# Performance work log

Measured on AMD Instinct MI355X. Metric: run time of the kernel, lower is better.

Reference implementation:

```python
import jax, jax.numpy as jnp
import numpy as np

HEADS = 8
DIM_HEAD = 64
NB_FEATURES = 256
DIM = 512

def setup_inputs() -> dict:
    key = jax.random.key(0)
    ks = jax.random.split(key, 4)
    b, n = 2, 8192
    x = jax.random.normal(ks[0], (b, n, DIM), jnp.float32)
    # fan-in scaling so exp(feature projections) stays numerically sane
    Wqkv = jax.random.normal(ks[1], (3 * HEADS * DIM_HEAD, DIM), jnp.float32) / np.sqrt(DIM).astype(np.float32)
    Wout = jax.random.normal(ks[2], (DIM, HEADS * DIM_HEAD), jnp.float32) / np.sqrt(HEADS * DIM_HEAD).astype(np.float32)
    bout = jnp.zeros((DIM,), jnp.float32)
    proj = jax.random.normal(ks[3], (NB_FEATURES, DIM_HEAD), jnp.float32) / np.sqrt(DIM_HEAD).astype(np.float32)
    return {"x": x, "Wqkv": Wqkv, "Wout": Wout, "bout": bout, "proj": proj}

def reference(x, Wqkv, Wout, bout, proj):
    b, n, _ = x.shape
    scale = DIM_HEAD ** -0.5
    qkv = jnp.einsum('bnd,ed->bne', x, Wqkv)            # [b,n,3*h*dh]
    q, k, v = jnp.split(qkv, 3, axis=-1)
    to_heads = lambda t: t.reshape(b, n, HEADS, DIM_HEAD).transpose(0, 2, 1, 3)  # [b,h,n,dh]
    q = to_heads(q) * scale
    k = to_heads(k)
    v = to_heads(v)
    # FAVOR+ exp feature maps
    q_prime = jnp.exp(jnp.einsum('bhnd,fd->bhnf', q, proj))  # [b,h,n,f]
    k_prime = jnp.exp(jnp.einsum('bhnd,fd->bhnf', k, proj))  # [b,h,n,f]
    k_sum = k_prime.sum(axis=2)                              # [b,h,f]
    D = jnp.einsum('bhnf,bhf->bhn', q_prime, k_sum)          # normalizer
    D_inv = 1.0 / (D + 1e-6)
    context = jnp.einsum('bhmf,bhmd->bhfd', k_prime, v)      # [b,h,f,dh]
    out = jnp.einsum('bhnf,bhfd->bhnd', q_prime, context) * D_inv[..., None]
    out = out.transpose(0, 2, 1, 3).reshape(b, n, HEADS * DIM_HEAD)
    return jnp.einsum('bne,de->bnd', out, Wout) + bout
```

## Files before the change

### kernel.cpp

```cpp
#include <hip/hip_runtime.h>
#include <math.h>

#define B_    2
#define NSEQ  8192
#define DIM_  512
#define H_    8
#define DH_   64
#define F_    256
#define M_    (B_*NSEQ)
#define QKV_  1536

typedef __attribute__((ext_vector_type(8))) short     short8;
typedef __attribute__((ext_vector_type(4))) float     float4v;
typedef __attribute__((ext_vector_type(8))) unsigned short ushort8v;

__device__ __forceinline__ unsigned short f2bf(float f) {
    unsigned u = __float_as_uint(f);
    u += 0x7FFFu + ((u >> 16) & 1u);
    return (unsigned short)(u >> 16);
}
__device__ __forceinline__ float bf2f(unsigned short h) {
    unsigned u = ((unsigned)h) << 16;
    return __uint_as_float(u);
}
__device__ __forceinline__ unsigned pack2bf(float lo, float hi) {
    return __builtin_amdgcn_perm(__float_as_uint(hi), __float_as_uint(lo), 0x07060302);
}
__device__ __forceinline__ void glds16(const void* g, void* s) {
    __builtin_amdgcn_global_load_lds(
        (const __attribute__((address_space(1))) unsigned int*)g,
        (__attribute__((address_space(3))) unsigned int*)s, 16, 0, 0);
}

__global__ __launch_bounds__(256) void cvt_all(const float* __restrict__ x,
                                               const float* __restrict__ wqkv,
                                               const float* __restrict__ wout,
                                               const float* __restrict__ proj,
                                               unsigned short* __restrict__ xb,
                                               unsigned short* __restrict__ wqkvb,
                                               unsigned short* __restrict__ woutb,
                                               unsigned short* __restrict__ projb) {
    int bid = blockIdx.x;
    const float* in; unsigned short* out; int i;
    if (bid < 4096)      { in = x;    out = xb;    i = bid * 256 + threadIdx.x; }
    else if (bid < 4480) { in = wqkv; out = wqkvb; i = (bid - 4096) * 256 + threadIdx.x; }
    else if (bid < 4608) { in = wout; out = woutb; i = (bid - 4480) * 256 + threadIdx.x; }
    else                 { in = proj; out = projb; i = (bid - 4608) * 256 + threadIdx.x; }
    float4 a = ((const float4*)in)[2 * i];
    float4 b = ((const float4*)in)[2 * i + 1];
    ushort8v o;
    o[0] = f2bf(a.x); o[1] = f2bf(a.y); o[2] = f2bf(a.z); o[3] = f2bf(a.w);
    o[4] = f2bf(b.x); o[5] = f2bf(b.y); o[6] = f2bf(b.z); o[7] = f2bf(b.w);
    ((ushort8v*)out)[i] = o;
}

template<bool BF16OUT>
__global__ __launch_bounds__(256) void gemm_nt_pp(const unsigned short* __restrict__ A,
                                                  const unsigned short* __restrict__ Bm,
                                                  const float* __restrict__ bias,
                                                  void* __restrict__ Cout,
                                                  unsigned short* __restrict__ vTout,
                                                  int M, int N, int K) {
    __shared__ __align__(16) unsigned short As[3][128 * 32];
    __shared__ __align__(16) unsigned short Bs[3][128 * 32];
    const int t  = threadIdx.x;
    const int w  = t >> 6, l = t & 63;
    const int wm = w >> 1, wn = w & 1;
    const int lr = l & 15, lq = l >> 4;

    const int gx = gridDim.x;
    int flat = blockIdx.y * gx + blockIdx.x;
    int per  = (gx * gridDim.y) >> 3;
    int flat2 = (flat & 7) * per + (flat >> 3);
    const int m0 = (flat2 / gx) * 128, n0 = (flat2 % gx) * 128;

    float4v acc[4][4];
#pragma unroll
    for (int mi = 0; mi < 4; mi++)
#pragma unroll
        for (int ni = 0; ni < 4; ni++) acc[mi][ni] = (float4v){0.f, 0.f, 0.f, 0.f};

    auto stage = [&](int buf, int k0) {
#pragma unroll
        for (int i = 0; i < 2; i++) {
            int rb8 = w * 2 + i;
            int row = rb8 * 16 + lr;
            glds16(A + (size_t)(m0 + row) * K + k0 + lq * 8, &As[buf][rb8 * 512]);
            glds16(Bm + (size_t)(n0 + row) * K + k0 + lq * 8, &Bs[buf][rb8 * 512]);
        }
    };

    const int nk = K >> 5;
    stage(0, 0);
    stage(1, 32);

    for (int k = 0; k < nk; k++) {
        if (k + 1 < nk) { asm volatile("s_waitcnt vmcnt(4)" ::: "memory"); }
        else            { asm volatile("s_waitcnt vmcnt(0)" ::: "memory"); }
        __builtin_amdgcn_s_barrier();

        const int cur = k % 3;
        if (k + 2 < nk) stage((k + 2) % 3, (k + 2) << 5);

        short8 af[4], bfr[4];
#pragma unroll
        for (int mi = 0; mi < 4; mi++)
            af[mi] = *(const short8*)&As[cur][((wm * 4 + mi) * 64 + l) * 8];
#pragma unroll
        for (int ni = 0; ni < 4; ni++)
            bfr[ni] = *(const short8*)&Bs[cur][((wn * 4 + ni) * 64 + l) * 8];

        __builtin_amdgcn_s_setprio(1);
#pragma unroll
        for (int mi = 0; mi < 4; mi++)
#pragma unroll
            for (int ni = 0; ni < 4; ni++)
                acc[mi][ni] = __builtin_amdgcn_mfma_f32_16x16x32_bf16(
                    af[mi], bfr[ni], acc[mi][ni], 0, 0, 0);
        __builtin_amdgcn_s_setprio(0);
    }

    const int q = l >> 4, c = l & 15;
#pragma unroll
    for (int mi = 0; mi < 4; mi++) {
        int row0 = m0 + wm * 64 + mi * 16 + q * 4;
#pragma unroll
        for (int ni = 0; ni < 4; ni++) {
            int col = n0 + wn * 64 + ni * 16 + c;
            if (BF16OUT && vTout != nullptr && col >= 1024) {
                int cm = col - 1024;
                int h2 = cm >> 6, dh = cm & 63;
                int bq = row0 >> 13;
                size_t nn = (size_t)(row0 & 8191);
                unsigned short* dst = vTout + (((size_t)bq * 8 + h2) * 64 + dh) * NSEQ + nn;
                uint2 pv;
                pv.x = ((unsigned)f2bf(acc[mi][ni][1]) << 16) | f2bf(acc[mi][ni][0]);
                pv.y = ((unsigned)f2bf(acc[mi][ni][3]) << 16) | f2bf(acc[mi][ni][2]);
                *(uint2*)dst = pv;
            } else {
                float bv = bias ? bias[col] : 0.f;
#pragma unroll
                for (int r = 0; r < 4; r++) {
                    float v = acc[mi][ni][r] + bv;
                    if (BF16OUT) ((unsigned short*)Cout)[(size_t)(row0 + r) * N + col] = f2bf(v);
                    else         ((float*)Cout)[(size_t)(row0 + r) * N + col] = v;
                }
            }
        }
    }
}

__global__ __launch_bounds__(512) void gemm_out_256(const unsigned short* __restrict__ A,
                                                    const unsigned short* __restrict__ Bm,
                                                    const float* __restrict__ bias,
                                                    float* __restrict__ Cout,
                                                    int M, int N, int K) {
    __shared__ __align__(16) unsigned short As[3][32 * 512];
    __shared__ __align__(16) unsigned short Bs[3][16 * 512];
    const int t  = threadIdx.x;
    const int w  = t >> 6, l = t & 63;
    const int wm = w >> 1, wn = w & 1;
    const int lr = l & 15, lq = l >> 4;

    const int gx = gridDim.x;
    int flat = blockIdx.y * gx + blockIdx.x;
    int per  = (gx * gridDim.y) >> 3;
    int flat2 = (flat & 7) * per + (flat >> 3);
    const int m0 = (flat2 / gx) * 256, n0 = (flat2 % gx) * 128;

    float4v acc[4][4];
#pragma unroll
    for (int mi = 0; mi < 4; mi++)
#pragma unroll
        for (int ni = 0; ni < 4; ni++) acc[mi][ni] = (float4v){0.f, 0.f, 0.f, 0.f};

    auto stage = [&](int buf, int k0) {
#pragma unroll
        for (int i = 0; i < 4; i++) {
            int c = w * 4 + i, rb = c >> 1, ks = c & 1;
            glds16(A + (size_t)(m0 + rb * 16 + lr) * K + k0 + ks * 32 + lq * 8,
                   &As[buf][c * 512]);
        }
#pragma unroll
        for (int i = 0; i < 2; i++) {
            int c = w * 2 + i, rb = c >> 1, ks = c & 1;
            glds16(Bm + (size_t)(n0 + rb * 16 + lr) * K + k0 + ks * 32 + lq * 8,
                   &Bs[buf][c * 512]);
        }
    };

    stage(0, 0);
    stage(1, 64);

#pragma unroll
    for (int k = 0; k < 8; k++) {
        if (k < 7) { asm volatile("s_waitcnt vmcnt(6)" ::: "memory"); }
        else       { asm volatile("s_waitcnt vmcnt(0)" ::: "memory"); }
        __builtin_amdgcn_s_barrier();
        const int cur = k % 3;

        if (k + 2 < 8) stage((k + 2) % 3, (k + 2) << 6);

        short8 af[2][4], bfr[2][4];
#pragma unroll
        for (int ks = 0; ks < 2; ks++) {
#pragma unroll
            for (int mi = 0; mi < 4; mi++)
                af[ks][mi] = *(const short8*)&As[cur][(((wm * 4 + mi) * 2 + ks) * 64 + l) * 8];
#pragma unroll
            for (int ni = 0; ni < 4; ni++)
                bfr[ks][ni] = *(const short8*)&Bs[cur][(((wn * 4 + ni) * 2 + ks) * 64 + l) * 8];
        }

        __builtin_amdgcn_s_setprio(1);
#pragma unroll
        for (int ks = 0; ks < 2; ks++)
#pragma unroll
            for (int mi = 0; mi < 4; mi++)
#pragma unroll
                for (int ni = 0; ni < 4; ni++)
                    acc[mi][ni] = __builtin_amdgcn_mfma_f32_16x16x32_bf16(
                        af[ks][mi], bfr[ks][ni], acc[mi][ni], 0, 0, 0);
        __builtin_amdgcn_s_setprio(0);
    }

    const int q = l >> 4, c = l & 15;
#pragma unroll
    for (int mi = 0; mi < 4; mi++) {
        int row0 = m0 + wm * 64 + mi * 16 + q * 4;
#pragma unroll
        for (int ni = 0; ni < 4; ni++) {
            int col = n0 + wn * 64 + ni * 16 + c;
            float bv = bias ? bias[col] : 0.f;
#pragma unroll
            for (int r = 0; r < 4; r++)
                Cout[(size_t)(row0 + r) * N + col] = acc[mi][ni][r] + bv;
        }
    }
}

__global__ __launch_bounds__(256) void ctx_fused_mfma(
    const unsigned short* __restrict__ qkvb,
    const unsigned short* __restrict__ projb,
    const unsigned short* __restrict__ vT,
    unsigned short* __restrict__ partial)
{
    __shared__ __align__(16) unsigned short PB[16 * 512];
    __shared__ __align__(16) unsigned short KB[8 * 512];
    __shared__ __align__(16) unsigned short VB[8 * 512];
    __shared__ __align__(16) unsigned short KPA[16 * 512];
    const int t = threadIdx.x, w = t >> 6, l = t & 63;
    const int lr = l & 15, lq = l >> 4;
    const int s = blockIdx.x, fh = blockIdx.y, z = blockIdx.z;
    const int b = z >> 3, h = z & 7;
    const int nchunk = s * 512;

    for (int idx = w; idx < 16; idx += 4) {
        int fblk = idx >> 1, kt = idx & 1;
        glds16(projb + (size_t)(fh * 128 + fblk * 16 + lr) * 64 + kt * 32 + lq * 8, &PB[idx * 512]);
    }

    float4v acc[2][5];
#pragma unroll
    for (int mi = 0; mi < 2; mi++)
#pragma unroll
        for (int ni = 0; ni < 5; ni++) acc[mi][ni] = (float4v){0.f, 0.f, 0.f, 0.f};
    short ov = (lr == 0) ? (short)0x3F80 : (short)0;
    short8 ones = {ov, ov, ov, ov, ov, ov, ov, ov};

    for (int st = 0; st < 8; st++) {
        int nbase = nchunk + st * 64;
        __syncthreads();
        for (int idx = w; idx < 8; idx += 4) {
            int nblk = idx >> 1, kt = idx & 1;
            glds16(qkvb + ((size_t)b * NSEQ + nbase + nblk * 16 + lr) * QKV_ + 512 + h * 64 + kt * 32 + lq * 8,
                   &KB[idx * 512]);
        }
        for (int idx = w; idx < 8; idx += 4) {
            int dhb = idx >> 1, nt2 = idx & 1;
            glds16(vT + ((size_t)z * 64 + dhb * 16 + lr) * NSEQ + nbase + nt2 * 32 + lq * 8,
                   &VB[idx * 512]);
        }
        __syncthreads();

        float4v a2[4][2];
#pragma unroll
        for (int mi = 0; mi < 4; mi++)
#pragma unroll
            for (int ni = 0; ni < 2; ni++) a2[mi][ni] = (float4v){0.f, 0.f, 0.f, 0.f};
#pragma unroll
        for (int ks = 0; ks < 2; ks++) {
            short8 ka[4], pb[2];
#pragma unroll
            for (int mi = 0; mi < 4; mi++)
                ka[mi] = *(const short8*)&KB[((mi * 2 + ks) * 64 + l) * 8];
#pragma unroll
            for (int ni = 0; ni < 2; ni++)
                pb[ni] = *(const short8*)&PB[(((w * 2 + ni) * 2 + ks) * 64 + l) * 8];
#pragma unroll
            for (int mi = 0; mi < 4; mi++)
#pragma unroll
                for (int ni = 0; ni < 2; ni++)
                    a2[mi][ni] = __builtin_amdgcn_mfma_f32_16x16x32_bf16(ka[mi], pb[ni], a2[mi][ni], 0, 0, 0);
        }
#pragma unroll
        for (int mi = 0; mi < 4; mi++) {
            int nb = mi * 16 + lq * 4;
            int qoff = ((nb >> 3) & 3) * 256 + (nb & 7) * 2;
            int setn = nb >> 5;
#pragma unroll
            for (int ni = 0; ni < 2; ni++) {
                int fp = w * 32 + ni * 16 + lr;
                float e0 = __expf(a2[mi][ni][0]);
                float e1 = __expf(a2[mi][ni][1]);
                float e2 = __expf(a2[mi][ni][2]);
                float e3 = __expf(a2[mi][ni][3]);
                uint2 p; p.x = pack2bf(e0, e1); p.y = pack2bf(e2, e3);
                *(uint2*)((char*)KPA + (size_t)(((fp >> 4) * 2 + setn) * 1024 + qoff + (fp & 15) * 16)) = p;
            }
        }
#pragma unroll
        for (int ks = 0; ks < 2; ks++) {
            short8 af[2], bf[4];
#pragma unroll
            for (int mi = 0; mi < 2; mi++)
                af[mi] = *(const short8*)&KPA[(((w * 2 + mi) * 2 + ks) * 64 + l) * 8];
#pragma unroll
            for (int ni = 0; ni < 4; ni++)
                bf[ni] = *(const short8*)&VB[((ni * 2 + ks) * 64 + l) * 8];
#pragma unroll
            for (int mi = 0; mi < 2; mi++) {
#pragma unroll
                for (int ni = 0; ni < 4; ni++)
                    acc[mi][ni] = __builtin_amdgcn_mfma_f32_16x16x32_bf16(af[mi], bf[ni], acc[mi][ni], 0, 0, 0);
                acc[mi][4] = __builtin_amdgcn_mfma_f32_16x16x32_bf16(af[mi], ones, acc[mi][4], 0, 0, 0);
            }
        }
    }
    unsigned short* base = partial + (size_t)(s * 16 + z) * 80 * 256 + fh * 128;
#pragma unroll
    for (int mi = 0; mi < 2; mi++) {
        int f0r = w * 32 + mi * 16 + lq * 4;
#pragma unroll
        for (int ni = 0; ni < 5; ni++) {
            int col = ni * 16 + lr;
#pragma unroll
            for (int r = 0; r < 4; r++)
                base[(size_t)col * 256 + f0r + r] = f2bf(acc[mi][ni][r]);
        }
    }
}

__global__ __launch_bounds__(256) void ctx_reduce(const unsigned short* __restrict__ partial,
                                                  unsigned short* __restrict__ ctxT) {
    int idx2 = blockIdx.x * 256 + threadIdx.x;
    const int INNER = 16 * 80 * 256;
    size_t off = (size_t)idx2 * 2;
    float s0 = 0.f, s1 = 0.f;
#pragma unroll
    for (int k = 0; k < 16; k++) {
        unsigned v = *(const unsigned*)(partial + (size_t)k * INNER + off);
        s0 += bf2f((unsigned short)(v & 0xffffu));
        s1 += bf2f((unsigned short)(v >> 16));
    }
    *(unsigned*)(ctxT + off) = ((unsigned)f2bf(s1) << 16) | f2bf(s0);
}

__global__ __launch_bounds__(256) void attn_fused_mfma(
    const unsigned short* __restrict__ qkvb,
    const unsigned short* __restrict__ projb,
    const unsigned short* __restrict__ ctxT,
    unsigned short* __restrict__ attnb)
{
    __shared__ __align__(16) unsigned short QB[16 * 512];
    __shared__ __align__(16) unsigned short PA[8 * 512];
    __shared__ __align__(16) unsigned short QPA[16 * 512];
    __shared__ __align__(16) unsigned short CB[10 * 512];
    const int t = threadIdx.x, w = t >> 6, l = t & 63;
    const int lr = l & 15, lq = l >> 4;
    const int m0 = blockIdx.x * 128, z = blockIdx.y;
    const int b = z >> 3, h = z & 7;

    for (int idx = w; idx < 16; idx += 4) {
        int mblk = idx >> 1, kt = idx & 1;
        glds16(qkvb + ((size_t)b * NSEQ + m0 + mblk * 16 + lr) * QKV_ + h * 64 + kt * 32 + lq * 8,
               &QB[idx * 512]);
    }
    float4v acc[2][5];
#pragma unroll
    for (int mi = 0; mi < 2; mi++)
#pragma unroll
        for (int ni = 0; ni < 5; ni++) acc[mi][ni] = (float4v){0.f, 0.f, 0.f, 0.f};

    for (int fs = 0; fs < 4; fs++) {
        int f0 = fs * 64;
        __syncthreads();
        for (int idx = w; idx < 8; idx += 4) {
            int fb = idx >> 1, kt = idx & 1;
            glds16(projb + (size_t)(f0 + fb * 16 + lr) * 64 + kt * 32 + lq * 8, &PA[idx * 512]);
        }
        for (int idx = w; idx < 10; idx += 4) {
            int dhb = idx >> 1, ft = idx & 1;
            glds16(ctxT + ((size_t)z * 80 + dhb * 16 + lr) * 256 + f0 + ft * 32 + lq * 8,
                   &CB[idx * 512]);
        }
        __syncthreads();

        float4v a2[4][2];
#pragma unroll
        for (int mi = 0; mi < 4; mi++)
#pragma unroll
            for (int ni = 0; ni < 2; ni++) a2[mi][ni] = (float4v){0.f, 0.f, 0.f, 0.f};
#pragma unroll
        for (int ks = 0; ks < 2; ks++) {
            short8 pa[4], qb[2];
#pragma unroll
            for (int mi = 0; mi < 4; mi++)
                pa[mi] = *(const short8*)&PA[((mi * 2 + ks) * 64 + l) * 8];
#pragma unroll
            for (int ni = 0; ni < 2; ni++)
                qb[ni] = *(const short8*)&QB[(((w * 2 + ni) * 2 + ks) * 64 + l) * 8];
#pragma unroll
            for (int mi = 0; mi < 4; mi++)
#pragma unroll
                for (int ni = 0; ni < 2; ni++)
                    a2[mi][ni] = __builtin_amdgcn_mfma_f32_16x16x32_bf16(pa[mi], qb[ni], a2[mi][ni], 0, 0, 0);
        }
#pragma unroll
        for (int mi = 0; mi < 4; mi++) {
            int fb2 = mi * 16 + lq * 4;
            int qoff = ((fb2 >> 3) & 3) * 256 + (fb2 & 7) * 2;
            int setf = fb2 >> 5;
#pragma unroll
            for (int ni = 0; ni < 2; ni++) {
                int m = w * 32 + ni * 16 + lr;
                float e0 = __expf(0.125f * a2[mi][ni][0]);
                float e1 = __expf(0.125f * a2[mi][ni][1]);
                float e2 = __expf(0.125f * a2[mi][ni][2]);
                float e3 = __expf(0.125f * a2[mi][ni][3]);
                uint2 p; p.x = pack2bf(e0, e1); p.y = pack2bf(e2, e3);
                *(uint2*)((char*)QPA + (size_t)(((m >> 4) * 2 + setf) * 1024 + qoff + (m & 15) * 16)) = p;
            }
        }
#pragma unroll
        for (int ks = 0; ks < 2; ks++) {
            short8 af[2], cb[5];
#pragma unroll
            for (int mi = 0; mi < 2; mi++)
                af[mi] = *(const short8*)&QPA[(((w * 2 + mi) * 2 + ks) * 64 + l) * 8];
#pragma unroll
            for (int ni = 0; ni < 5; ni++)
                cb[ni] = *(const short8*)&CB[((ni * 2 + ks) * 64 + l) * 8];
#pragma unroll
            for (int mi = 0; mi < 2; mi++)
#pragma unroll
                for (int ni = 0; ni < 5; ni++)
                    acc[mi][ni] = __builtin_amdgcn_mfma_f32_16x16x32_bf16(af[mi], cb[ni], acc[mi][ni], 0, 0, 0);
        }
    }
#pragma unroll
    for (int mi = 0; mi < 2; mi++) {
        int rowb = m0 + w * 32 + mi * 16 + lq * 4;
#pragma unroll
        for (int r = 0; r < 4; r++) {
            float dv = __shfl(acc[mi][4][r], (l & 48), 64);
            float rinv = 1.f / (dv + 1e-6f);
#pragma unroll
            for (int ni = 0; ni < 4; ni++)
                attnb[((size_t)b * NSEQ + rowb + r) * 512 + h * 64 + ni * 16 + lr] =
                    f2bf(acc[mi][ni][r] * rinv);
        }
    }
}

extern "C" void kernel_launch(void* const* d_in, const int* in_sizes, int n_in,
                              void* d_out, int out_size, void* d_ws, size_t ws_size,
                              hipStream_t stream) {
    const float* x    = (const float*)d_in[0];
    const float* Wqkv = (const float*)d_in[1];
    const float* Wout = (const float*)d_in[2];
    const float* bout = (const float*)d_in[3];
    const float* proj = (const float*)d_in[4];

    unsigned short* qkvb    = (unsigned short*)d_ws;
    unsigned short* vT      = qkvb + (size_t)M_ * QKV_;
    unsigned short* partial = vT + (size_t)16 * 64 * NSEQ;
    unsigned short* ctxT    = partial + (size_t)16 * 16 * 80 * 256;
    unsigned short* projb   = ctxT + (size_t)16 * 80 * 256;
    unsigned short* xb      = projb + 16384;
    unsigned short* attnb   = xb;
    unsigned short* wqkvb   = xb + (size_t)M_ * DIM_;
    unsigned short* woutb   = wqkvb + (size_t)QKV_ * DIM_;
    float* outp = (float*)d_out;

    cvt_all<<<dim3(4616), 256, 0, stream>>>(x, Wqkv, Wout, proj, xb, wqkvb, woutb, projb);
    gemm_nt_pp<true><<<dim3(QKV_ / 128, M_ / 128), 256, 0, stream>>>(xb, wqkvb, nullptr, qkvb, vT, M_, QKV_, DIM_);
    ctx_fused_mfma<<<dim3(16, 2, 16), 256, 0, stream>>>(qkvb, projb, vT, partial);
    ctx_reduce<<<dim3(640), 256, 0, stream>>>(partial, ctxT);
    attn_fused_mfma<<<dim3(64, 16), 256, 0, stream>>>(qkvb, projb, ctxT, attnb);
    gemm_out_256<<<dim3(DIM_ / 128, M_ / 256), 512, 0, stream>>>(attnb, woutb, bout, outp, M_, DIM_, DIM_);
}
```

Before: 211.4 us.

## Deepen GEMM pipeline to five stages and double-buffer attention kernel loads

The GEMM kernel moves from a 3-buffer to a 5-buffer LDS ring, prefetching four K-tiles ahead with adjusted vmcnt waits. The context and output attention kernels double-buffer their K/V and proj/ctx tiles, so the next chunk's global-to-LDS copy is issued while the current chunk is computed. This is meant to hide global memory latency, at the cost of more shared memory per block, which may lower occupancy. In the attention kernels the wait is still vmcnt(0) at the top of each iteration, so the overlap reaches only across one compute phase.

```diff
diff --git a/kernel.cpp b/kernel.cpp
--- a/kernel.cpp
+++ b/kernel.cpp
@@ -61,8 +61,8 @@
                                                   void* __restrict__ Cout,
                                                   unsigned short* __restrict__ vTout,
                                                   int M, int N, int K) {
-    __shared__ __align__(16) unsigned short As[3][128 * 32];
-    __shared__ __align__(16) unsigned short Bs[3][128 * 32];
+    __shared__ __align__(16) unsigned short As[5][128 * 32];
+    __shared__ __align__(16) unsigned short Bs[5][128 * 32];
     const int t  = threadIdx.x;
     const int w  = t >> 6, l = t & 63;
     const int wm = w >> 1, wn = w & 1;
@@ -93,14 +93,18 @@
     const int nk = K >> 5;
     stage(0, 0);
     stage(1, 32);
+    stage(2, 64);
+    stage(3, 96);
 
     for (int k = 0; k < nk; k++) {
-        if (k + 1 < nk) { asm volatile("s_waitcnt vmcnt(4)" ::: "memory"); }
-        else            { asm volatile("s_waitcnt vmcnt(0)" ::: "memory"); }
+        if (k + 3 < nk)      { asm volatile("s_waitcnt vmcnt(12)" ::: "memory"); }
+        else if (k + 2 < nk) { asm volatile("s_waitcnt vmcnt(8)"  ::: "memory"); }
+        else if (k + 1 < nk) { asm volatile("s_waitcnt vmcnt(4)"  ::: "memory"); }
+        else                 { asm volatile("s_waitcnt vmcnt(0)"  ::: "memory"); }
         __builtin_amdgcn_s_barrier();
 
-        const int cur = k % 3;
-        if (k + 2 < nk) stage((k + 2) % 3, (k + 2) << 5);
+        const int cur = k % 5;
+        if (k + 4 < nk) stage((k + 4) % 5, (k + 4) << 5);
 
         short8 af[4], bfr[4];
 #pragma unroll
@@ -246,8 +250,8 @@
     unsigned short* __restrict__ partial)
 {
     __shared__ __align__(16) unsigned short PB[16 * 512];
-    __shared__ __align__(16) unsigned short KB[8 * 512];
-    __shared__ __align__(16) unsigned short VB[8 * 512];
+    __shared__ __align__(16) unsigned short KB[2][8 * 512];
+    __shared__ __align__(16) unsigned short VB[2][8 * 512];
     __shared__ __align__(16) unsigned short KPA[16 * 512];
     const int t = threadIdx.x, w = t >> 6, l = t & 63;
     const int lr = l & 15, lq = l >> 4;
@@ -255,10 +259,24 @@
     const int b = z >> 3, h = z & 7;
     const int nchunk = s * 512;
 
+    auto stageKV = [&](int bi, int nbase) {
+        for (int idx = w; idx < 8; idx += 4) {
+            int nblk = idx >> 1, kt = idx & 1;
+            glds16(qkvb + ((size_t)b * NSEQ + nbase + nblk * 16 + lr) * QKV_ + 512 + h * 64 + kt * 32 + lq * 8,
+                   &KB[bi][idx * 512]);
+        }
+        for (int idx = w; idx < 8; idx += 4) {
+            int dhb = idx >> 1, nt2 = idx & 1;
+            glds16(vT + ((size_t)z * 64 + dhb * 16 + lr) * NSEQ + nbase + nt2 * 32 + lq * 8,
+                   &VB[bi][idx * 512]);
+        }
+    };
+
     for (int idx = w; idx < 16; idx += 4) {
         int fblk = idx >> 1, kt = idx & 1;
         glds16(projb + (size_t)(fh * 128 + fblk * 16 + lr) * 64 + kt * 32 + lq * 8, &PB[idx * 512]);
     }
+    stageKV(0, nchunk);
 
     float4v acc[2][5];
 #pragma unroll
@@ -269,19 +287,11 @@
     short8 ones = {ov, ov, ov, ov, ov, ov, ov, ov};
 
     for (int st = 0; st < 8; st++) {
-        int nbase = nchunk + st * 64;
-        __syncthreads();
-        for (int idx = w; idx < 8; idx += 4) {
-            int nblk = idx >> 1, kt = idx & 1;
-            glds16(qkvb + ((size_t)b * NSEQ + nbase + nblk * 16 + lr) * QKV_ + 512 + h * 64 + kt * 32 + lq * 8,
-                   &KB[idx * 512]);
-        }
-        for (int idx = w; idx < 8; idx += 4) {
-            int dhb = idx >> 1, nt2 = idx & 1;
-            glds16(vT + ((size_t)z * 64 + dhb * 16 + lr) * NSEQ + nbase + nt2 * 32 + lq * 8,
-                   &VB[idx * 512]);
-        }
-        __syncthreads();
+        asm volatile("s_waitcnt vmcnt(0)" ::: "memory");
+        __builtin_amdgcn_s_barrier();
+        asm volatile("" ::: "memory");
+        const int cur = st & 1;
+        if (st < 7) stageKV(cur ^ 1, nchunk + (st + 1) * 64);
 
         float4v a2[4][2];
 #pragma unroll
@@ -293,7 +303,7 @@
             short8 ka[4], pb[2];
 #pragma unroll
             for (int mi = 0; mi < 4; mi++)
-                ka[mi] = *(const short8*)&KB[((mi * 2 + ks) * 64 + l) * 8];
+                ka[mi] = *(const short8*)&KB[cur][((mi * 2 + ks) * 64 + l) * 8];
 #pragma unroll
             for (int ni = 0; ni < 2; ni++)
                 pb[ni] = *(const short8*)&PB[(((w * 2 + ni) * 2 + ks) * 64 + l) * 8];
@@ -327,7 +337,7 @@
                 af[mi] = *(const short8*)&KPA[(((w * 2 + mi) * 2 + ks) * 64 + l) * 8];
 #pragma unroll
             for (int ni = 0; ni < 4; ni++)
-                bf[ni] = *(const short8*)&VB[((ni * 2 + ks) * 64 + l) * 8];
+                bf[ni] = *(const short8*)&VB[cur][((ni * 2 + ks) * 64 + l) * 8];
 #pragma unroll
             for (int mi = 0; mi < 2; mi++) {
 #pragma unroll
@@ -373,19 +383,33 @@
     unsigned short* __restrict__ attnb)
 {
     __shared__ __align__(16) unsigned short QB[16 * 512];
-    __shared__ __align__(16) unsigned short PA[8 * 512];
+    __shared__ __align__(16) unsigned short PA[2][8 * 512];
     __shared__ __align__(16) unsigned short QPA[16 * 512];
-    __shared__ __align__(16) unsigned short CB[10 * 512];
+    __shared__ __align__(16) unsigned short CB[2][10 * 512];
     const int t = threadIdx.x, w = t >> 6, l = t & 63;
     const int lr = l & 15, lq = l >> 4;
     const int m0 = blockIdx.x * 128, z = blockIdx.y;
     const int b = z >> 3, h = z & 7;
 
+    auto stagePC = [&](int bi, int f0n) {
+        for (int idx = w; idx < 8; idx += 4) {
+            int fb = idx >> 1, kt = idx & 1;
+            glds16(projb + (size_t)(f0n + fb * 16 + lr) * 64 + kt * 32 + lq * 8, &PA[bi][idx * 512]);
+        }
+        for (int idx = w; idx < 10; idx += 4) {
+            int dhb = idx >> 1, ft = idx & 1;
+            glds16(ctxT + ((size_t)z * 80 + dhb * 16 + lr) * 256 + f0n + ft * 32 + lq * 8,
+                   &CB[bi][idx * 512]);
+        }
+    };
+
     for (int idx = w; idx < 16; idx += 4) {
         int mblk = idx >> 1, kt = idx & 1;
         glds16(qkvb + ((size_t)b * NSEQ + m0 + mblk * 16 + lr) * QKV_ + h * 64 + kt * 32 + lq * 8,
                &QB[idx * 512]);
     }
+    stagePC(0, 0);
+
     float4v acc[2][5];
 #pragma unroll
     for (int mi = 0; mi < 2; mi++)
@@ -393,18 +417,11 @@
         for (int ni = 0; ni < 5; ni++) acc[mi][ni] = (float4v){0.f, 0.f, 0.f, 0.f};
 
     for (int fs = 0; fs < 4; fs++) {
-        int f0 = fs * 64;
-        __syncthreads();
-        for (int idx = w; idx < 8; idx += 4) {
-            int fb = idx >> 1, kt = idx & 1;
-            glds16(projb + (size_t)(f0 + fb * 16 + lr) * 64 + kt * 32 + lq * 8, &PA[idx * 512]);
-        }
-        for (int idx = w; idx < 10; idx += 4) {
-            int dhb = idx >> 1, ft = idx & 1;
-            glds16(ctxT + ((size_t)z * 80 + dhb * 16 + lr) * 256 + f0 + ft * 32 + lq * 8,
-                   &CB[idx * 512]);
-        }
-        __syncthreads();
+        asm volatile("s_waitcnt vmcnt(0)" ::: "memory");
+        __builtin_amdgcn_s_barrier();
+        asm volatile("" ::: "memory");
+        const int cur = fs & 1;
+        if (fs < 3) stagePC(cur ^ 1, (fs + 1) * 64);
 
         float4v a2[4][2];
 #pragma unroll
@@ -416,7 +433,7 @@
             short8 pa[4], qb[2];
 #pragma unroll
             for (int mi = 0; mi < 4; mi++)
-                pa[mi] = *(const short8*)&PA[((mi * 2 + ks) * 64 + l) * 8];
+                pa[mi] = *(const short8*)&PA[cur][((mi * 2 + ks) * 64 + l) * 8];
 #pragma unroll
             for (int ni = 0; ni < 2; ni++)
                 qb[ni] = *(const short8*)&QB[(((w * 2 + ni) * 2 + ks) * 64 + l) * 8];
@@ -450,7 +467,7 @@
                 af[mi] = *(const short8*)&QPA[(((w * 2 + mi) * 2 + ks) * 64 + l) * 8];
 #pragma unroll
             for (int ni = 0; ni < 5; ni++)
-                cb[ni] = *(const short8*)&CB[((ni * 2 + ks) * 64 + l) * 8];
+                cb[ni] = *(const short8*)&CB[cur][((ni * 2 + ks) * 64 + l) * 8];
 #pragma unroll
             for (int mi = 0; mi < 2; mi++)
 #pragma unroll
```

Measured after the change: 216.8 us. 1.03x slower.
